# Optimization experiments

Measured on AMD Instinct MI355X. Metric: run time of the kernel, lower is better.

Reference implementation:

```python
import jax, jax.numpy as jnp
import numpy as np

V, H, O = 32, 256, 256  # input_dim, hidden_dim, output_dim
EPS = 1e-5


def _layer_norm(x, g, b):
    m = jnp.mean(x, axis=-1, keepdims=True)
    v = jnp.mean((x - m) ** 2, axis=-1, keepdims=True)
    return g * (x - m) * jax.lax.rsqrt(v + EPS) + b


def setup_inputs() -> dict:
    key = jax.random.key(0)
    ks = jax.random.split(key, 20)
    s = 0.05
    inp = {
        "x": jax.random.normal(ks[0], (16, 256, V), dtype=jnp.float32),
        # selection GRN (input_dim -> input_dim, identity skip)
        "sel_fc1_w": jax.random.normal(ks[1], (V, H), dtype=jnp.float32) * s,
        "sel_fc1_b": jnp.zeros((H,), jnp.float32),
        "sel_fc2_w": jax.random.normal(ks[2], (H, V), dtype=jnp.float32) * s,
        "sel_fc2_b": jnp.zeros((V,), jnp.float32),
        "sel_gate_w": jax.random.normal(ks[3], (V, 2 * V), dtype=jnp.float32) * s,
        "sel_gate_b": jnp.zeros((2 * V,), jnp.float32),
        "sel_ln_g": jnp.ones((V,), jnp.float32),
        "sel_ln_b": jnp.zeros((V,), jnp.float32),
        # per-variable GRNs, stacked over the V variables (each has in_dim=1)
        "var_fc1_w": jax.random.normal(ks[4], (V, H), dtype=jnp.float32) * s,
        "var_fc1_b": jnp.zeros((V, H), jnp.float32),
        "var_fc2_w": jax.random.normal(ks[5], (V, H, O), dtype=jnp.float32) * s,
        "var_fc2_b": jnp.zeros((V, O), jnp.float32),
        "var_gate_w": jax.random.normal(ks[6], (V, 2 * O), dtype=jnp.float32) * s,
        "var_gate_b": jnp.zeros((V, 2 * O), jnp.float32),
        "var_skip_w": jax.random.normal(ks[7], (V, O), dtype=jnp.float32) * s,
        "var_skip_b": jnp.zeros((V, O), jnp.float32),
        "var_ln_g": jnp.ones((V, O), jnp.float32),
        "var_ln_b": jnp.zeros((V, O), jnp.float32),
    }
    return inp


def _vsn_forward(x, sel_fc1_w, sel_fc1_b, sel_fc2_w, sel_fc2_b, sel_gate_w,
                 sel_gate_b, sel_ln_g, sel_ln_b, var_fc1_w, var_fc1_b,
                 var_fc2_w, var_fc2_b, var_gate_w, var_gate_b, var_skip_w,
                 var_skip_b, var_ln_g, var_ln_b):
    B, S, _ = x.shape
    xr = x.reshape(-1, V)  # [N, V]

    # --- selection GRN (skip is identity) ---
    h = jax.nn.elu(xr @ sel_fc1_w + sel_fc1_b)        # [N, H]
    h = h @ sel_fc2_w + sel_fc2_b                      # [N, V] (unused by residual; matches torch code)
    g = xr @ sel_gate_w + sel_gate_b                   # [N, 2V]
    gates, values = jnp.split(g, 2, axis=-1)
    glu = jax.nn.sigmoid(gates) * values               # [N, V]
    sel = _layer_norm(glu + xr, sel_ln_g, sel_ln_b)    # [N, V]
    weights = jax.nn.softmax(sel, axis=-1)             # [N, V]

    # --- batched per-variable GRNs (in_dim = 1) ---
    xv = xr[..., None]                                  # [N, V, 1]
    hv = jax.nn.elu(xv * var_fc1_w + var_fc1_b)         # [N, V, H]
    hv = jnp.einsum('nvh,vho->nvo', hv, var_fc2_w) + var_fc2_b  # [N, V, O]
    gv = xv * var_gate_w + var_gate_b                   # [N, V, 2O]
    gates_v, values_v = jnp.split(gv, 2, axis=-1)
    glu_v = jax.nn.sigmoid(gates_v) * values_v          # [N, V, O]
    skip_v = xv * var_skip_w + var_skip_b               # [N, V, O]
    proc = _layer_norm(glu_v + skip_v, var_ln_g, var_ln_b)  # [N, V, O]

    out = jnp.einsum('nv,nvo->no', weights, proc)       # [N, O]
    return out.reshape(B, S, O)


def reference(x, sel_fc1_w, sel_fc1_b, sel_fc2_w, sel_fc2_b, sel_gate_w,
              sel_gate_b, sel_ln_g, sel_ln_b, var_fc1_w, var_fc1_b,
              var_fc2_w, var_fc2_b, var_gate_w, var_gate_b, var_skip_w,
              var_skip_b, var_ln_g, var_ln_b):
    return _vsn_forward(x, sel_fc1_w, sel_fc1_b, sel_fc2_w, sel_fc2_b,
                        sel_gate_w, sel_gate_b, sel_ln_g, sel_ln_b,
                        var_fc1_w, var_fc1_b, var_fc2_w, var_fc2_b,
                        var_gate_w, var_gate_b, var_skip_w, var_skip_b,
                        var_ln_g, var_ln_b)
```

## Files before the change

kernel.cpp:

```cpp
#include <hip/hip_runtime.h>
#include <hip/hip_bf16.h>


#define VDIM 32
#define ODIM 256
#define RPB  16
#define TPB  512
#define NL2E (-1.4426950408889634f)

template <int CTRL>
__device__ __forceinline__ float dpp_add(float x) {
    int s = __builtin_amdgcn_update_dpp(0, __builtin_bit_cast(int, x),
                                        CTRL, 0xF, 0xF, true);
    return x + __builtin_bit_cast(float, s);
}

__device__ __forceinline__ float wave_sum(float x) {
    x = dpp_add<0x111>(x);
    x = dpp_add<0x112>(x);
    x = dpp_add<0x114>(x);
    x = dpp_add<0x118>(x);
    x = dpp_add<0x142>(x);
    x = dpp_add<0x143>(x);
    return __builtin_bit_cast(float,
        __builtin_amdgcn_readlane(__builtin_bit_cast(int, x), 63));
}

__device__ __forceinline__ float fast_sigmoid(float g) {
    return __builtin_amdgcn_rcpf(1.0f + __expf(-g));
}

__device__ __forceinline__ unsigned bf16rne(float f) {
    unsigned u = __builtin_bit_cast(unsigned, f);
    return (u + 0x7FFFu + ((u >> 16) & 1u)) >> 16;
}
__device__ __forceinline__ unsigned pack2(float lo, float hi) {
    return bf16rne(lo) | (bf16rne(hi) << 16);
}

#define BFLO(u) __builtin_bit_cast(float, (u) << 16)
#define BFHI(u) __builtin_bit_cast(float, (u) & 0xFFFF0000u)

__global__ void __launch_bounds__(TPB) vsn_fused(
    const float* __restrict__ x,
    const float* __restrict__ sgw,
    const float* __restrict__ sgb,
    const float* __restrict__ slg,
    const float* __restrict__ slb,
    const float* __restrict__ vgw,
    const float* __restrict__ vgb,
    const float* __restrict__ vsw,
    const float* __restrict__ vsb,
    const float* __restrict__ vlg,
    const float* __restrict__ vlb,
    float* __restrict__ out)
{
    __shared__ unsigned short wlds[32 * 2048];
    __shared__ float2 xw_s[RPB][VDIM];
    __shared__ float  g_s[RPB][2 * VDIM];

    const int tid  = threadIdx.x;
    const int row0 = blockIdx.x * RPB;

    xw_s[tid >> 5][tid & 31].x = x[row0 * VDIM + tid];

    {
        const int r = tid >> 1, h = tid & 1;
        const int v = r >> 3, a = r & 7;
        const float* src;
        if (a == 0)      src = vgw + v * 512;
        else if (a == 1) src = vgw + v * 512 + 256;
        else if (a == 2) src = vgb + v * 512;
        else if (a == 3) src = vgb + v * 512 + 256;
        else if (a == 4) src = vsw + v * 256;
        else if (a == 5) src = vsb + v * 256;
        else if (a == 6) src = vlg + v * 256;
        else             src = vlb + v * 256;
        src += h * 128;
        const float scale = (a == 0 || a == 2) ? NL2E : 1.0f;
        unsigned short* dst = wlds + v * 2048 + a * 256 + h * 128;
        #pragma unroll 4
        for (int i = 0; i < 16; ++i) {
            const float4 f0 = *(const float4*)(src + i * 8);
            const float4 f1 = *(const float4*)(src + i * 8 + 4);
            uint4 p;
            p.x = pack2(f0.x * scale, f0.y * scale);
            p.y = pack2(f0.z * scale, f0.w * scale);
            p.z = pack2(f1.x * scale, f1.y * scale);
            p.w = pack2(f1.z * scale, f1.w * scale);
            *(uint4*)(dst + i * 8) = p;
        }
    }
    __syncthreads();

    #pragma unroll
    for (int it = 0; it < 2; ++it) {
        const int i = tid + it * TPB;
        const int r = i >> 6, j = i & 63;
        float acc = sgb[j];
        #pragma unroll
        for (int v = 0; v < VDIM; ++v)
            acc = fmaf(xw_s[r][v].x, sgw[v * 64 + j], acc);
        g_s[r][j] = acc;
    }
    __syncthreads();

    {
        const int r = tid >> 5, v = tid & 31;
        const float gate = g_s[r][v];
        const float val  = g_s[r][VDIM + v];
        const float y    = fast_sigmoid(gate) * val + xw_s[r][v].x;
        float s1 = y, s2 = y * y;
        #pragma unroll
        for (int m = 1; m < 32; m <<= 1) {
            s1 += __shfl_xor(s1, m, 64);
            s2 += __shfl_xor(s2, m, 64);
        }
        const float mean = s1 * (1.0f / VDIM);
        const float var  = s2 * (1.0f / VDIM) - mean * mean;
        const float rs   = __builtin_amdgcn_rsqf(var + 1e-5f);
        const float sel  = slg[v] * ((y - mean) * rs) + slb[v];
        float mx = sel;
        #pragma unroll
        for (int m = 1; m < 32; m <<= 1)
            mx = fmaxf(mx, __shfl_xor(mx, m, 64));
        const float e = __expf(sel - mx);
        float se = e;
        #pragma unroll
        for (int m = 1; m < 32; m <<= 1)
            se += __shfl_xor(se, m, 64);
        xw_s[r][v].y = e * __builtin_amdgcn_rcpf(se);
    }
    __syncthreads();

    const int wave = tid >> 6;
    const int lane = tid & 63;
    const int o0   = lane << 2;
    const int rA   = wave * 2, rB = rA + 1;

    float aA0 = 0.f, aA1 = 0.f, aA2 = 0.f, aA3 = 0.f;
    float aB0 = 0.f, aB1 = 0.f, aB2 = 0.f, aB3 = 0.f;

    #pragma unroll 2
    for (int v = 0; v < VDIM; ++v) {
        const unsigned short* wv = wlds + v * 2048 + o0;
        const uint2 Ugw = *(const uint2*)(wv);
        const uint2 Uvw = *(const uint2*)(wv + 256);
        const uint2 Ugb = *(const uint2*)(wv + 512);
        const uint2 Uvb = *(const uint2*)(wv + 768);
        const uint2 Usw = *(const uint2*)(wv + 1024);
        const uint2 Usb = *(const uint2*)(wv + 1280);
        const uint2 Ulg = *(const uint2*)(wv + 1536);
        const uint2 Ulb = *(const uint2*)(wv + 1792);
        const float2 XA = xw_s[rA][v];
        const float2 XB = xw_s[rB][v];
        const float xa = XA.x, wa = XA.y, xb = XB.x, wb = XB.y;

        const float gw0 = BFLO(Ugw.x), gw1 = BFHI(Ugw.x), gw2 = BFLO(Ugw.y), gw3 = BFHI(Ugw.y);
        const float vw0 = BFLO(Uvw.x), vw1 = BFHI(Uvw.x), vw2 = BFLO(Uvw.y), vw3 = BFHI(Uvw.y);
        const float gb0 = BFLO(Ugb.x), gb1 = BFHI(Ugb.x), gb2 = BFLO(Ugb.y), gb3 = BFHI(Ugb.y);
        const float vb0 = BFLO(Uvb.x), vb1 = BFHI(Uvb.x), vb2 = BFLO(Uvb.y), vb3 = BFHI(Uvb.y);
        const float sw0 = BFLO(Usw.x), sw1 = BFHI(Usw.x), sw2 = BFLO(Usw.y), sw3 = BFHI(Usw.y);
        const float sb0 = BFLO(Usb.x), sb1 = BFHI(Usb.x), sb2 = BFLO(Usb.y), sb3 = BFHI(Usb.y);
        const float lg0 = BFLO(Ulg.x), lg1 = BFHI(Ulg.x), lg2 = BFLO(Ulg.y), lg3 = BFHI(Ulg.y);
        const float lb0 = BFLO(Ulb.x), lb1 = BFHI(Ulb.x), lb2 = BFLO(Ulb.y), lb3 = BFHI(Ulb.y);

        #define YV(xr, k) fmaf(__builtin_amdgcn_rcpf(1.0f + \
            __builtin_amdgcn_exp2f(fmaf(xr, gw##k, gb##k))), \
            fmaf(xr, vw##k, vb##k), fmaf(xr, sw##k, sb##k))
        const float yA0 = YV(xa, 0), yA1 = YV(xa, 1), yA2 = YV(xa, 2), yA3 = YV(xa, 3);
        const float yB0 = YV(xb, 0), yB1 = YV(xb, 1), yB2 = YV(xb, 2), yB3 = YV(xb, 3);
        #undef YV

        const float s1a = wave_sum((yA0 + yA1) + (yA2 + yA3));
        const float s2a = wave_sum(fmaf(yA0, yA0, fmaf(yA1, yA1, fmaf(yA2, yA2, yA3 * yA3))));
        const float s1b = wave_sum((yB0 + yB1) + (yB2 + yB3));
        const float s2b = wave_sum(fmaf(yB0, yB0, fmaf(yB1, yB1, fmaf(yB2, yB2, yB3 * yB3))));

        const float mA  = s1a * (1.0f / ODIM);
        const float vA  = s2a * (1.0f / ODIM) - mA * mA;
        const float rsA = __builtin_amdgcn_rsqf(vA + 1e-5f);
        const float wrsA = wa * rsA;
        aA0 = fmaf(lg0, (yA0 - mA) * wrsA, fmaf(wa, lb0, aA0));
        aA1 = fmaf(lg1, (yA1 - mA) * wrsA, fmaf(wa, lb1, aA1));
        aA2 = fmaf(lg2, (yA2 - mA) * wrsA, fmaf(wa, lb2, aA2));
        aA3 = fmaf(lg3, (yA3 - mA) * wrsA, fmaf(wa, lb3, aA3));

        const float mB  = s1b * (1.0f / ODIM);
        const float vB  = s2b * (1.0f / ODIM) - mB * mB;
        const float rsB = __builtin_amdgcn_rsqf(vB + 1e-5f);
        const float wrsB = wb * rsB;
        aB0 = fmaf(lg0, (yB0 - mB) * wrsB, fmaf(wb, lb0, aB0));
        aB1 = fmaf(lg1, (yB1 - mB) * wrsB, fmaf(wb, lb1, aB1));
        aB2 = fmaf(lg2, (yB2 - mB) * wrsB, fmaf(wb, lb2, aB2));
        aB3 = fmaf(lg3, (yB3 - mB) * wrsB, fmaf(wb, lb3, aB3));
    }

    *(float4*)(out + (size_t)(row0 + rA) * ODIM + o0) = make_float4(aA0, aA1, aA2, aA3);
    *(float4*)(out + (size_t)(row0 + rB) * ODIM + o0) = make_float4(aB0, aB1, aB2, aB3);
}

extern "C" void kernel_launch(void* const* d_in, const int* in_sizes, int n_in,
                              void* d_out, int out_size, void* d_ws, size_t ws_size,
                              hipStream_t stream) {
    const float* x   = (const float*)d_in[0];
    const float* sgw = (const float*)d_in[5];
    const float* sgb = (const float*)d_in[6];
    const float* slg = (const float*)d_in[7];
    const float* slb = (const float*)d_in[8];
    const float* vgw = (const float*)d_in[13];
    const float* vgb = (const float*)d_in[14];
    const float* vsw = (const float*)d_in[15];
    const float* vsb = (const float*)d_in[16];
    const float* vlg = (const float*)d_in[17];
    const float* vlb = (const float*)d_in[18];
    float* out = (float*)d_out;

    const int N = in_sizes[0] / VDIM;
    const int grid = N / RPB;

    vsn_fused<<<grid, TPB, 0, stream>>>(x, sgw, sgb, slg, slb,
                                        vgw, vgb, vsw, vsb, vlg, vlb, out);
}
```

Measured before the change: 133.9 us.

## Interleave variable pairs in bf16 LDS weight layout for wider loads

Changes the shared-memory weight layout so each 32-bit word packs the bf16 values of two adjacent variables at the same output column. The main loop then runs over 16 variable pairs with 128-bit LDS loads, halving the number of LDS load instructions and exposing more independent work per iteration. The weight staging is also rewritten as a coalesced, fully unrolled pass over the whole block, and the x/weight scratch becomes float4 per variable pair. The cost is higher register pressure from the larger unrolled body, which may lower occupancy.

Result: faster. 124.1 us (-7.3%).

```diff
diff --git a/kernel.cpp b/kernel.cpp
--- a/kernel.cpp
+++ b/kernel.cpp
@@ -34,8 +34,8 @@
     unsigned u = __builtin_bit_cast(unsigned, f);
     return (u + 0x7FFFu + ((u >> 16) & 1u)) >> 16;
 }
-__device__ __forceinline__ unsigned pack2(float lo, float hi) {
-    return bf16rne(lo) | (bf16rne(hi) << 16);
+__device__ __forceinline__ unsigned packvv(float a, float b) {
+    return bf16rne(a) | (bf16rne(b) << 16);
 }
 
 #define BFLO(u) __builtin_bit_cast(float, (u) << 16)
@@ -55,41 +55,44 @@
     const float* __restrict__ vlb,
     float* __restrict__ out)
 {
-    __shared__ unsigned short wlds[32 * 2048];
-    __shared__ float2 xw_s[RPB][VDIM];
+    __shared__ unsigned wlds[16 * 2048];
+    __shared__ float4 xw_s[RPB][16];
     __shared__ float  g_s[RPB][2 * VDIM];
 
     const int tid  = threadIdx.x;
     const int row0 = blockIdx.x * RPB;
 
-    xw_s[tid >> 5][tid & 31].x = x[row0 * VDIM + tid];
-
     {
-        const int r = tid >> 1, h = tid & 1;
-        const int v = r >> 3, a = r & 7;
-        const float* src;
-        if (a == 0)      src = vgw + v * 512;
-        else if (a == 1) src = vgw + v * 512 + 256;
-        else if (a == 2) src = vgb + v * 512;
-        else if (a == 3) src = vgb + v * 512 + 256;
-        else if (a == 4) src = vsw + v * 256;
-        else if (a == 5) src = vsb + v * 256;
-        else if (a == 6) src = vlg + v * 256;
-        else             src = vlb + v * 256;
-        src += h * 128;
-        const float scale = (a == 0 || a == 2) ? NL2E : 1.0f;
-        unsigned short* dst = wlds + v * 2048 + a * 256 + h * 128;
-        #pragma unroll 4
-        for (int i = 0; i < 16; ++i) {
-            const float4 f0 = *(const float4*)(src + i * 8);
-            const float4 f1 = *(const float4*)(src + i * 8 + 4);
-            uint4 p;
-            p.x = pack2(f0.x * scale, f0.y * scale);
-            p.y = pack2(f0.z * scale, f0.w * scale);
-            p.z = pack2(f1.x * scale, f1.y * scale);
-            p.w = pack2(f1.z * scale, f1.w * scale);
-            *(uint4*)(dst + i * 8) = p;
-        }
+        const int r = tid >> 5, v = tid & 31;
+        ((float*)&xw_s[r][v >> 1])[(v & 1) << 1] = x[row0 * VDIM + tid];
+    }
+
+    #pragma unroll
+    for (int k = 0; k < 16; ++k) {
+        const int c = k * TPB + tid;
+        const int p = c >> 9;
+        const int a = (c >> 6) & 7;
+        const int o = (c & 63) << 2;
+        const int vA = p * 2, vB = vA + 1;
+        const float* sA;
+        const float* sB;
+        if (a == 0)      { sA = vgw + vA * 512;       sB = vgw + vB * 512; }
+        else if (a == 1) { sA = vgw + vA * 512 + 256; sB = vgw + vB * 512 + 256; }
+        else if (a == 2) { sA = vgb + vA * 512;       sB = vgb + vB * 512; }
+        else if (a == 3) { sA = vgb + vA * 512 + 256; sB = vgb + vB * 512 + 256; }
+        else if (a == 4) { sA = vsw + vA * 256;       sB = vsw + vB * 256; }
+        else if (a == 5) { sA = vsb + vA * 256;       sB = vsb + vB * 256; }
+        else if (a == 6) { sA = vlg + vA * 256;       sB = vlg + vB * 256; }
+        else             { sA = vlb + vA * 256;       sB = vlb + vB * 256; }
+        const float4 fA = *(const float4*)(sA + o);
+        const float4 fB = *(const float4*)(sB + o);
+        const float s = (a == 0 || a == 2) ? NL2E : 1.0f;
+        uint4 P;
+        P.x = packvv(fA.x * s, fB.x * s);
+        P.y = packvv(fA.y * s, fB.y * s);
+        P.z = packvv(fA.z * s, fB.z * s);
+        P.w = packvv(fA.w * s, fB.w * s);
+        ((uint4*)wlds)[c] = P;
     }
     __syncthreads();
 
@@ -100,16 +103,18 @@
         float acc = sgb[j];
         #pragma unroll
         for (int v = 0; v < VDIM; ++v)
-            acc = fmaf(xw_s[r][v].x, sgw[v * 64 + j], acc);
+            acc = fmaf(((const float*)&xw_s[r][v >> 1])[(v & 1) << 1],
+                       sgw[v * 64 + j], acc);
         g_s[r][j] = acc;
     }
     __syncthreads();
 
     {
         const int r = tid >> 5, v = tid & 31;
+        const float xv   = ((const float*)&xw_s[r][v >> 1])[(v & 1) << 1];
         const float gate = g_s[r][v];
         const float val  = g_s[r][VDIM + v];
-        const float y    = fast_sigmoid(gate) * val + xw_s[r][v].x;
+        const float y    = fast_sigmoid(gate) * val + xv;
         float s1 = y, s2 = y * y;
         #pragma unroll
         for (int m = 1; m < 32; m <<= 1) {
@@ -129,7 +134,8 @@
         #pragma unroll
         for (int m = 1; m < 32; m <<= 1)
             se += __shfl_xor(se, m, 64);
-        xw_s[r][v].y = e * __builtin_amdgcn_rcpf(se);
+        ((float*)&xw_s[r][v >> 1])[((v & 1) << 1) + 1] =
+            e * __builtin_amdgcn_rcpf(se);
     }
     __syncthreads();
 
@@ -141,59 +147,90 @@
     float aA0 = 0.f, aA1 = 0.f, aA2 = 0.f, aA3 = 0.f;
     float aB0 = 0.f, aB1 = 0.f, aB2 = 0.f, aB3 = 0.f;
 
-    #pragma unroll 2
-    for (int v = 0; v < VDIM; ++v) {
-        const unsigned short* wv = wlds + v * 2048 + o0;
-        const uint2 Ugw = *(const uint2*)(wv);
-        const uint2 Uvw = *(const uint2*)(wv + 256);
-        const uint2 Ugb = *(const uint2*)(wv + 512);
-        const uint2 Uvb = *(const uint2*)(wv + 768);
-        const uint2 Usw = *(const uint2*)(wv + 1024);
-        const uint2 Usb = *(const uint2*)(wv + 1280);
-        const uint2 Ulg = *(const uint2*)(wv + 1536);
-        const uint2 Ulb = *(const uint2*)(wv + 1792);
-        const float2 XA = xw_s[rA][v];
-        const float2 XB = xw_s[rB][v];
-        const float xa = XA.x, wa = XA.y, xb = XB.x, wb = XB.y;
-
-        const float gw0 = BFLO(Ugw.x), gw1 = BFHI(Ugw.x), gw2 = BFLO(Ugw.y), gw3 = BFHI(Ugw.y);
-        const float vw0 = BFLO(Uvw.x), vw1 = BFHI(Uvw.x), vw2 = BFLO(Uvw.y), vw3 = BFHI(Uvw.y);
-        const float gb0 = BFLO(Ugb.x), gb1 = BFHI(Ugb.x), gb2 = BFLO(Ugb.y), gb3 = BFHI(Ugb.y);
-        const float vb0 = BFLO(Uvb.x), vb1 = BFHI(Uvb.x), vb2 = BFLO(Uvb.y), vb3 = BFHI(Uvb.y);
-        const float sw0 = BFLO(Usw.x), sw1 = BFHI(Usw.x), sw2 = BFLO(Usw.y), sw3 = BFHI(Usw.y);
-        const float sb0 = BFLO(Usb.x), sb1 = BFHI(Usb.x), sb2 = BFLO(Usb.y), sb3 = BFHI(Usb.y);
-        const float lg0 = BFLO(Ulg.x), lg1 = BFHI(Ulg.x), lg2 = BFLO(Ulg.y), lg3 = BFHI(Ulg.y);
-        const float lb0 = BFLO(Ulb.x), lb1 = BFHI(Ulb.x), lb2 = BFLO(Ulb.y), lb3 = BFHI(Ulb.y);
-
-        #define YV(xr, k) fmaf(__builtin_amdgcn_rcpf(1.0f + \
-            __builtin_amdgcn_exp2f(fmaf(xr, gw##k, gb##k))), \
-            fmaf(xr, vw##k, vb##k), fmaf(xr, sw##k, sb##k))
-        const float yA0 = YV(xa, 0), yA1 = YV(xa, 1), yA2 = YV(xa, 2), yA3 = YV(xa, 3);
-        const float yB0 = YV(xb, 0), yB1 = YV(xb, 1), yB2 = YV(xb, 2), yB3 = YV(xb, 3);
-        #undef YV
-
-        const float s1a = wave_sum((yA0 + yA1) + (yA2 + yA3));
-        const float s2a = wave_sum(fmaf(yA0, yA0, fmaf(yA1, yA1, fmaf(yA2, yA2, yA3 * yA3))));
-        const float s1b = wave_sum((yB0 + yB1) + (yB2 + yB3));
-        const float s2b = wave_sum(fmaf(yB0, yB0, fmaf(yB1, yB1, fmaf(yB2, yB2, yB3 * yB3))));
-
-        const float mA  = s1a * (1.0f / ODIM);
-        const float vA  = s2a * (1.0f / ODIM) - mA * mA;
-        const float rsA = __builtin_amdgcn_rsqf(vA + 1e-5f);
-        const float wrsA = wa * rsA;
-        aA0 = fmaf(lg0, (yA0 - mA) * wrsA, fmaf(wa, lb0, aA0));
-        aA1 = fmaf(lg1, (yA1 - mA) * wrsA, fmaf(wa, lb1, aA1));
-        aA2 = fmaf(lg2, (yA2 - mA) * wrsA, fmaf(wa, lb2, aA2));
-        aA3 = fmaf(lg3, (yA3 - mA) * wrsA, fmaf(wa, lb3, aA3));
-
-        const float mB  = s1b * (1.0f / ODIM);
-        const float vB  = s2b * (1.0f / ODIM) - mB * mB;
-        const float rsB = __builtin_amdgcn_rsqf(vB + 1e-5f);
-        const float wrsB = wb * rsB;
-        aB0 = fmaf(lg0, (yB0 - mB) * wrsB, fmaf(wb, lb0, aB0));
-        aB1 = fmaf(lg1, (yB1 - mB) * wrsB, fmaf(wb, lb1, aB1));
-        aB2 = fmaf(lg2, (yB2 - mB) * wrsB, fmaf(wb, lb2, aB2));
-        aB3 = fmaf(lg3, (yB3 - mB) * wrsB, fmaf(wb, lb3, aB3));
+    for (int p = 0; p < 16; ++p) {
+        const unsigned* wv = wlds + (p << 11) + o0;
+        const uint4 Ugw = *(const uint4*)(wv);
+        const uint4 Uvw = *(const uint4*)(wv + 256);
+        const uint4 Ugb = *(const uint4*)(wv + 512);
+        const uint4 Uvb = *(const uint4*)(wv + 768);
+        const uint4 Usw = *(const uint4*)(wv + 1024);
+        const uint4 Usb = *(const uint4*)(wv + 1280);
+        const uint4 Ulg = *(const uint4*)(wv + 1536);
+        const uint4 Ulb = *(const uint4*)(wv + 1792);
+        const float4 XA = xw_s[rA][p];
+        const float4 XB = xw_s[rB][p];
+
+        float yA[2][4], yB[2][4];
+        #define UW(U, k) ((k) == 0 ? U.x : (k) == 1 ? U.y : (k) == 2 ? U.z : U.w)
+        #pragma unroll
+        for (int k = 0; k < 4; ++k) {
+            const unsigned ugw = UW(Ugw, k), uvw = UW(Uvw, k), ugb = UW(Ugb, k),
+                           uvb = UW(Uvb, k), usw = UW(Usw, k), usb = UW(Usb, k);
+            {
+                const float gw = BFLO(ugw), vw = BFLO(uvw), gb = BFLO(ugb),
+                            vb = BFLO(uvb), sw = BFLO(usw), sb = BFLO(usb);
+                const float sgA = __builtin_amdgcn_rcpf(
+                    1.0f + __builtin_amdgcn_exp2f(fmaf(XA.x, gw, gb)));
+                yA[0][k] = fmaf(sgA, fmaf(XA.x, vw, vb), fmaf(XA.x, sw, sb));
+                const float sgB = __builtin_amdgcn_rcpf(
+                    1.0f + __builtin_amdgcn_exp2f(fmaf(XB.x, gw, gb)));
+                yB[0][k] = fmaf(sgB, fmaf(XB.x, vw, vb), fmaf(XB.x, sw, sb));
+            }
+            {
+                const float gw = BFHI(ugw), vw = BFHI(uvw), gb = BFHI(ugb),
+                            vb = BFHI(uvb), sw = BFHI(usw), sb = BFHI(usb);
+                const float sgA = __builtin_amdgcn_rcpf(
+                    1.0f + __builtin_amdgcn_exp2f(fmaf(XA.z, gw, gb)));
+                yA[1][k] = fmaf(sgA, fmaf(XA.z, vw, vb), fmaf(XA.z, sw, sb));
+                const float sgB = __builtin_amdgcn_rcpf(
+                    1.0f + __builtin_amdgcn_exp2f(fmaf(XB.z, gw, gb)));
+                yB[1][k] = fmaf(sgB, fmaf(XB.z, vw, vb), fmaf(XB.z, sw, sb));
+            }
+        }
+
+        const float s1A0 = wave_sum((yA[0][0] + yA[0][1]) + (yA[0][2] + yA[0][3]));
+        const float s2A0 = wave_sum(fmaf(yA[0][0], yA[0][0], fmaf(yA[0][1], yA[0][1],
+                                    fmaf(yA[0][2], yA[0][2], yA[0][3] * yA[0][3]))));
+        const float s1A1 = wave_sum((yA[1][0] + yA[1][1]) + (yA[1][2] + yA[1][3]));
+        const float s2A1 = wave_sum(fmaf(yA[1][0], yA[1][0], fmaf(yA[1][1], yA[1][1],
+                                    fmaf(yA[1][2], yA[1][2], yA[1][3] * yA[1][3]))));
+        const float s1B0 = wave_sum((yB[0][0] + yB[0][1]) + (yB[0][2] + yB[0][3]));
+        const float s2B0 = wave_sum(fmaf(yB[0][0], yB[0][0], fmaf(yB[0][1], yB[0][1],
+                                    fmaf(yB[0][2], yB[0][2], yB[0][3] * yB[0][3]))));
+        const float s1B1 = wave_sum((yB[1][0] + yB[1][1]) + (yB[1][2] + yB[1][3]));
+        const float s2B1 = wave_sum(fmaf(yB[1][0], yB[1][0], fmaf(yB[1][1], yB[1][1],
+                                    fmaf(yB[1][2], yB[1][2], yB[1][3] * yB[1][3]))));
+
+        #pragma unroll
+        for (int j = 0; j < 2; ++j) {
+            const float s1a = j ? s1A1 : s1A0, s2a = j ? s2A1 : s2A0;
+            const float s1b = j ? s1B1 : s1B0, s2b = j ? s2B1 : s2B0;
+            const float wa = j ? XA.w : XA.y;
+            const float wb = j ? XB.w : XB.y;
+
+            const float mA  = s1a * (1.0f / ODIM);
+            const float vA  = s2a * (1.0f / ODIM) - mA * mA;
+            const float wrsA = wa * __builtin_amdgcn_rsqf(vA + 1e-5f);
+            const float mwA = mA * wrsA;
+            const float mB  = s1b * (1.0f / ODIM);
+            const float vB  = s2b * (1.0f / ODIM) - mB * mB;
+            const float wrsB = wb * __builtin_amdgcn_rsqf(vB + 1e-5f);
+            const float mwB = mB * wrsB;
+
+            #define LG(k) (j ? BFHI(UW(Ulg, k)) : BFLO(UW(Ulg, k)))
+            #define LB(k) (j ? BFHI(UW(Ulb, k)) : BFLO(UW(Ulb, k)))
+            aA0 = fmaf(LG(0), fmaf(yA[j][0], wrsA, -mwA), fmaf(wa, LB(0), aA0));
+            aA1 = fmaf(LG(1), fmaf(yA[j][1], wrsA, -mwA), fmaf(wa, LB(1), aA1));
+            aA2 = fmaf(LG(2), fmaf(yA[j][2], wrsA, -mwA), fmaf(wa, LB(2), aA2));
+            aA3 = fmaf(LG(3), fmaf(yA[j][3], wrsA, -mwA), fmaf(wa, LB(3), aA3));
+            aB0 = fmaf(LG(0), fmaf(yB[j][0], wrsB, -mwB), fmaf(wb, LB(0), aB0));
+            aB1 = fmaf(LG(1), fmaf(yB[j][1], wrsB, -mwB), fmaf(wb, LB(1), aB1));
+            aB2 = fmaf(LG(2), fmaf(yB[j][2], wrsB, -mwB), fmaf(wb, LB(2), aB2));
+            aB3 = fmaf(LG(3), fmaf(yB[j][3], wrsB, -mwB), fmaf(wb, LB(3), aB3));
+            #undef LG
+            #undef LB
+        }
+        #undef UW
     }
 
     *(float4*)(out + (size_t)(row0 + rA) * ODIM + o0) = make_float4(aA0, aA1, aA2, aA3);
```
